# Kernel optimization log

Measured on AMD Instinct MI355X. Metric: run time of the kernel, lower is better.

## Reference

```python
import jax, jax.numpy as jnp
import numpy as np

B, A, D, H = 32, 64, 128, 512
F = A * D  # 8192

def setup_inputs() -> dict:
    key = jax.random.key(0)
    ks = jax.random.split(key, 20)
    s = 0.02
    return {
        "swarm_states": jax.random.normal(ks[0], (B, A, D), jnp.float32),
        "swarm_goals": jax.random.normal(ks[1], (B, A, D), jnp.float32),
        # quantum layer stand-in: Linear(F->F) + tanh
        "Wq": jax.random.normal(ks[2], (F, F), jnp.float32) * s,
        "bq": jnp.zeros((F,), jnp.float32),
        # interaction_net: Linear(2D->H) ReLU Linear(H->H) ReLU Linear(H->D)
        "Wi1": jax.random.normal(ks[3], (2 * D, H), jnp.float32) * s,
        "bi1": jnp.zeros((H,), jnp.float32),
        "Wi2": jax.random.normal(ks[4], (H, H), jnp.float32) * s,
        "bi2": jnp.zeros((H,), jnp.float32),
        "Wi3": jax.random.normal(ks[5], (H, D), jnp.float32) * s,
        "bi3": jnp.zeros((D,), jnp.float32),
        # coordination_net: Linear(F->H) ReLU Linear(H->H) ReLU Linear(H->F)
        "Wc1": jax.random.normal(ks[6], (F, H), jnp.float32) * s,
        "bc1": jnp.zeros((H,), jnp.float32),
        "Wc2": jax.random.normal(ks[7], (H, H), jnp.float32) * s,
        "bc2": jnp.zeros((H,), jnp.float32),
        "Wc3": jax.random.normal(ks[8], (H, F), jnp.float32) * s,
        "bc3": jnp.zeros((F,), jnp.float32),
    }

def reference(swarm_states, swarm_goals, Wq, bq, Wi1, bi1, Wi2, bi2, Wi3, bi3,
              Wc1, bc1, Wc2, bc2, Wc3, bc3):
    b, a, d = swarm_states.shape
    states_flat = swarm_states.reshape(b, a * d)
    # quantum feature extraction (stand-in for QuantumNeuralLayer)
    quantum_features = jnp.tanh(states_flat @ Wq + bq)  # (B, A*D)

    # vectorized pairwise interaction MLP over all ordered (i, j) pairs
    xi = jnp.broadcast_to(swarm_states[:, :, None, :], (b, a, a, d))
    xj = jnp.broadcast_to(swarm_states[:, None, :, :], (b, a, a, d))
    pair = jnp.concatenate([xi, xj], axis=-1)            # (B, A, A, 2D)
    h = jax.nn.relu(pair @ Wi1 + bi1)
    h = jax.nn.relu(h @ Wi2 + bi2)
    inter = h @ Wi3 + bi3                                # (B, A, A, D)
    offdiag = (1.0 - jnp.eye(a, dtype=inter.dtype))[None, :, :, None]
    # per-agent aggregation over the other agents (mean over j != i)
    interactions = (inter * offdiag).sum(axis=2) / (a - 1)  # (B, A, D)

    c = jax.nn.relu(quantum_features @ Wc1 + bc1)
    c = jax.nn.relu(c @ Wc2 + bc2)
    coordination = (c @ Wc3 + bc3).reshape(b, a, d)      # (B, A, D)

    coordinated_states = swarm_states + 0.1 * interactions + 0.1 * coordination
    return coordinated_states, quantum_features, interactions, coordination
```

## Files before the change

### kernel.cpp

```cpp
#include <hip/hip_runtime.h>

typedef __attribute__((ext_vector_type(8))) short bf16x8;
typedef __attribute__((ext_vector_type(16))) float f32x16;
typedef _Float16 f16;
typedef __attribute__((ext_vector_type(8))) _Float16 f16x8;

static __device__ __forceinline__ unsigned short f2bf(float x) {
  unsigned int u = __float_as_uint(x);
  return (unsigned short)((u + 0x7FFFu + ((u >> 16) & 1u)) >> 16);
}
static __device__ __forceinline__ unsigned int pk2bf(float lo, float hi) {
  return ((unsigned int)f2bf(hi) << 16) | f2bf(lo);
}

static __device__ __forceinline__ f16x8 relu8(f16x8 x) {
  f16x8 z = {0, 0, 0, 0, 0, 0, 0, 0};
  return __builtin_elementwise_max(x, z);
}

__global__ __launch_bounds__(256) void tobf_kernel(const float* __restrict__ src,
                                                   unsigned short* __restrict__ dst) {
  const int idx = blockIdx.x * 256 + threadIdx.x;
  float4 v = ((const float4*)src)[idx];
  ushort4 o;
  o.x = f2bf(v.x); o.y = f2bf(v.y); o.z = f2bf(v.z); o.w = f2bf(v.w);
  ((ushort4*)dst)[idx] = o;
}

__global__ __launch_bounds__(256) void w2h_kernel(const float* __restrict__ Wi2,
                                                  f16* __restrict__ W2h) {
  __shared__ float tile[32][33];
  const int t = threadIdx.x;
  const int bk = blockIdx.x, bn = blockIdx.y;
  const int r = t >> 5, c = t & 31;
#pragma unroll
  for (int p = 0; p < 4; p++) {
    int rr = p * 8 + r;
    tile[rr][c] = Wi2[(bk * 32 + rr) * 512 + bn * 32 + c];
  }
  __syncthreads();
#pragma unroll
  for (int p = 0; p < 4; p++) {
    int rr = p * 8 + r;
    W2h[(bn * 32 + rr) * 512 + bk * 32 + c] = (f16)tile[c][rr];
  }
}

__global__ __launch_bounds__(256) void uvh_kernel(const float* __restrict__ S,
                                                  const float* __restrict__ Wi1,
                                                  const float* __restrict__ bi1,
                                                  f16* __restrict__ Uh, f16* __restrict__ Vg) {
  __shared__ float st[128][12];
  const int t = threadIdx.x;
  const int row0 = blockIdx.x * 8;
  for (int idx = t; idx < 1024; idx += 256) {
    int r = idx >> 7, k = idx & 127;
    st[k][r] = S[(row0 + r) * 128 + k];
  }
  __syncthreads();
  float au0[8], au1[8], av0[8], av1[8];
#pragma unroll
  for (int r = 0; r < 8; r++) { au0[r] = 0.f; au1[r] = 0.f; av0[r] = 0.f; av1[r] = 0.f; }
#pragma unroll 4
  for (int k = 0; k < 128; k++) {
    float wt0 = Wi1[k * 512 + t];
    float wt1 = Wi1[k * 512 + 256 + t];
    float wb0 = Wi1[(k + 128) * 512 + t];
    float wb1 = Wi1[(k + 128) * 512 + 256 + t];
    float4 sA = *(const float4*)&st[k][0];
    float4 sB = *(const float4*)&st[k][4];
    float s8[8] = {sA.x, sA.y, sA.z, sA.w, sB.x, sB.y, sB.z, sB.w};
#pragma unroll
    for (int r = 0; r < 8; r++) {
      au0[r] += s8[r] * wt0;
      au1[r] += s8[r] * wt1;
      av0[r] += s8[r] * wb0;
      av1[r] += s8[r] * wb1;
    }
  }
  const float b0 = bi1[t], b1 = bi1[256 + t];
  const int kb = t >> 3, rem = t & 7;
#pragma unroll
  for (int r = 0; r < 8; r++) {
    const int row = row0 + r;
    Uh[row * 512 + t]       = (f16)(au0[r] + b0);
    Uh[row * 512 + 256 + t] = (f16)(au1[r] + b1);
    const int j = row & 63, bb = row >> 6;
    Vg[bb * 32768 + kb * 512 + j * 8 + rem]          = (f16)av0[r];
    Vg[bb * 32768 + (kb + 32) * 512 + j * 8 + rem]   = (f16)av1[r];
  }
}

__global__ __launch_bounds__(256, 4) void gemmw(const unsigned short* __restrict__ Abf,
                                                const float* __restrict__ W,
                                                float* __restrict__ P,
                                                int K, int N, int L, int l4sh) {
  __shared__ __align__(16) unsigned short As[32 * 512];
  const int t = threadIdx.x;
  const int k0 = blockIdx.y * L;
  const int L4 = L >> 2;
  const int swzm = 2 * L - 1;
  for (int idx = t; idx < (L << 3); idx += 256) {
    int row = idx >> l4sh, k4 = idx & (L4 - 1);
    ushort4 a4 = *(const ushort4*)&Abf[(size_t)row * K + k0 + k4 * 4];
    int off = (row * 2 * L + k4 * 8) ^ (((row & 7) << 4) & swzm);
    *(ushort4*)((char*)As + off) = a4;
  }
  __syncthreads();
  const int lane = t & 63, w = t >> 6;
  const int lrow = lane & 31, lh = lane >> 5;
  const int col = blockIdx.x * 128 + w * 32 + lrow;
  f32x16 acc0, acc1;
#pragma unroll
  for (int r = 0; r < 16; r++) { acc0[r] = 0.f; acc1[r] = 0.f; }
  const float* Wp = W + (size_t)(k0 + lh * 8) * N + col;
  const int aswz = ((lrow & 7) << 4) & swzm;
  const int abase = lrow * 2 * L + lh * 16;
  const int nks = L >> 4;
  int ks = 0;
  for (; ks + 1 < nks; ks += 2) {
    float wv0[8], wv1[8];
#pragma unroll
    for (int jj = 0; jj < 8; jj++) wv0[jj] = Wp[(size_t)(ks * 16 + jj) * N];
#pragma unroll
    for (int jj = 0; jj < 8; jj++) wv1[jj] = Wp[(size_t)(ks * 16 + 16 + jj) * N];
    uint4 b0, b1;
    b0.x = pk2bf(wv0[0], wv0[1]); b0.y = pk2bf(wv0[2], wv0[3]);
    b0.z = pk2bf(wv0[4], wv0[5]); b0.w = pk2bf(wv0[6], wv0[7]);
    b1.x = pk2bf(wv1[0], wv1[1]); b1.y = pk2bf(wv1[2], wv1[3]);
    b1.z = pk2bf(wv1[4], wv1[5]); b1.w = pk2bf(wv1[6], wv1[7]);
    bf16x8 af0 = *(const bf16x8*)((const char*)As + ((abase + ks * 32) ^ aswz));
    bf16x8 af1 = *(const bf16x8*)((const char*)As + ((abase + ks * 32 + 32) ^ aswz));
    acc0 = __builtin_amdgcn_mfma_f32_32x32x16_bf16(af0, *(const bf16x8*)&b0, acc0, 0, 0, 0);
    acc1 = __builtin_amdgcn_mfma_f32_32x32x16_bf16(af1, *(const bf16x8*)&b1, acc1, 0, 0, 0);
  }
  if (ks < nks) {
    float wv0[8];
#pragma unroll
    for (int jj = 0; jj < 8; jj++) wv0[jj] = Wp[(size_t)(ks * 16 + jj) * N];
    uint4 b0;
    b0.x = pk2bf(wv0[0], wv0[1]); b0.y = pk2bf(wv0[2], wv0[3]);
    b0.z = pk2bf(wv0[4], wv0[5]); b0.w = pk2bf(wv0[6], wv0[7]);
    bf16x8 af0 = *(const bf16x8*)((const char*)As + ((abase + ks * 32) ^ aswz));
    acc0 = __builtin_amdgcn_mfma_f32_32x32x16_bf16(af0, *(const bf16x8*)&b0, acc0, 0, 0, 0);
  }
  float* Pr = P + (size_t)blockIdx.y * 32 * N + col;
#pragma unroll
  for (int r = 0; r < 16; r++) {
    int row = (r & 3) + 8 * (r >> 2) + 4 * lh;
    Pr[(size_t)row * N] = acc0[r] + acc1[r];
  }
}

__global__ __launch_bounds__(256) void reduce_kernel(const float* __restrict__ P,
                                                     const float* __restrict__ bias,
                                                     float* __restrict__ dst,
                                                     unsigned short* __restrict__ dstbf,
                                                     int lnN, int KS, int act, int wbf) {
  const int idx = blockIdx.x * 256 + threadIdx.x;
  const int N = 1 << lnN;
  const int m = idx >> lnN, n = idx & (N - 1);
  float s = 0.f;
#pragma unroll 8
  for (int p = 0; p < KS; p++) s += P[((size_t)(p * 32 + m) << lnN) + n];
  s += bias[n];
  if (act == 1) s = fmaxf(s, 0.f);
  else if (act == 2) s = tanhf(s);
  dst[idx] = s;
  if (wbf) dstbf[idx] = f2bf(s);
}

__global__ __launch_bounds__(512, 2) void inter7_kernel(const f16* __restrict__ Uh,
                                                        const f16* __restrict__ Vg,
                                                        const f16* __restrict__ W2h,
                                                        const float* __restrict__ bi2,
                                                        float* __restrict__ Hsum) {
  __shared__ __align__(16) f16 Bt[128 * 512];
  const int t = threadIdx.x;
  const int nq = blockIdx.x;

#pragma unroll
  for (int i = 0; i < 16; i++) {
    int idx = i * 512 + t;
    int n = idx >> 6, ch = idx & 63;
    f16x8 w8 = *(const f16x8*)&W2h[(size_t)(nq * 128 + n) * 512 + ch * 8];
    int off = (n * 1024 + ch * 16) ^ ((n & 15) << 4);
    *(f16x8*)((char*)Bt + off) = w8;
  }
  __syncthreads();

  const int w = t >> 6, lane = t & 63;
  const int ii = w & 1, tg = w >> 1;
  const int lrow = lane & 31, lh = lane >> 5;
  const char* Btc = (const char*)Bt;

  int bofs[4], bswz[4];
#pragma unroll
  for (int nf = 0; nf < 4; nf++) {
    int nr = nf * 32 + lrow;
    bofs[nf] = nr * 1024 + lh * 16;
    bswz[nf] = (nr & 15) << 4;
  }

  const int b = blockIdx.y >> 1;
  const f16* Vbase = Vg + (size_t)b * 32768 + lh * 512 + lrow * 8;

  for (int s = 0; s < 4; s++) {
    const int tid = blockIdx.y * 16 + tg * 4 + s;
    const int it = tid & 31;
    const f16* Ub = Uh + (size_t)(b * 64 + it * 2 + ii) * 512 + lh * 8;

    f32x16 acc[2][4];
#pragma unroll
    for (int mf = 0; mf < 2; mf++)
#pragma unroll
      for (int nf = 0; nf < 4; nf++)
#pragma unroll
        for (int r = 0; r < 16; r++) acc[mf][nf][r] = 0.f;

    f16x8 v0 = *(const f16x8*)(Vbase);
    f16x8 v1 = *(const f16x8*)(Vbase + 256);
    f16x8 u0 = *(const f16x8*)(Ub);
    f16x8 bf[4];
#pragma unroll
    for (int nf = 0; nf < 4; nf++) bf[nf] = *(const f16x8*)(Btc + (bofs[nf] ^ bswz[nf]));

#pragma unroll 4
    for (int kc = 0; kc < 512; kc += 16) {
      const int kn = (kc + 16) & 511;
      f16x8 v0n = *(const f16x8*)(Vbase + kn * 64);
      f16x8 v1n = *(const f16x8*)(Vbase + kn * 64 + 256);
      f16x8 u0n = *(const f16x8*)(Ub + kn);
      f16x8 bfn[4];
#pragma unroll
      for (int nf = 0; nf < 4; nf++)
        bfn[nf] = *(const f16x8*)(Btc + ((bofs[nf] + kn * 2) ^ bswz[nf]));
      f16x8 a0 = relu8(v0 + u0);
      f16x8 a1 = relu8(v1 + u0);
#pragma unroll
      for (int nf = 0; nf < 4; nf++) {
        acc[0][nf] = __builtin_amdgcn_mfma_f32_32x32x16_f16(a0, bf[nf], acc[0][nf], 0, 0, 0);
        acc[1][nf] = __builtin_amdgcn_mfma_f32_32x32x16_f16(a1, bf[nf], acc[1][nf], 0, 0, 0);
      }
      v0 = v0n; v1 = v1n; u0 = u0n;
#pragma unroll
      for (int nf = 0; nf < 4; nf++) bf[nf] = bfn[nf];
    }

    const int iglob = it * 2 + ii;
    const int mf_d = iglob >> 5;
    const int rd = iglob & 31;
    const int lh_d = (rd >> 2) & 1;
    const int r_d = (rd & 3) + 4 * (rd >> 3);
#pragma unroll
    for (int nf = 0; nf < 4; nf++) {
      const int col = nq * 128 + nf * 32 + lrow;
      const float b2 = bi2[col];
      float ssum = 0.f;
#pragma unroll
      for (int mf = 0; mf < 2; mf++)
#pragma unroll
        for (int r = 0; r < 16; r++) {
          float x = fmaxf(acc[mf][nf][r] + b2, 0.f);
          if (mf == mf_d && r == r_d && lh == lh_d) x = 0.f;
          ssum += x;
        }
      ssum += __shfl_xor(ssum, 32);
      if (lh == 0) Hsum[(size_t)(b * 64 + iglob) * 512 + col] = ssum;
    }
  }
}

__global__ __launch_bounds__(256) void k3_kernel(const float* __restrict__ Hsum,
                                                 const float* __restrict__ Wi3,
                                                 const float* __restrict__ bi3,
                                                 float* __restrict__ inter) {
  __shared__ float st[512][10];
  const int t = threadIdx.x;
  const int row0 = blockIdx.x * 8;
  for (int idx = t; idx < 4096; idx += 256) {
    int r = idx >> 9, k = idx & 511;
    st[k][r] = Hsum[(row0 + r) * 512 + k] * (1.0f / 63.0f);
  }
  __syncthreads();
  const int c = t & 63;
  const int rg = t >> 6;
  float a0[2] = {0.f, 0.f}, a1[2] = {0.f, 0.f};
#pragma unroll 4
  for (int k = 0; k < 512; k++) {
    float w0 = Wi3[k * 128 + c];
    float w1 = Wi3[k * 128 + 64 + c];
    float2 h = *(const float2*)&st[k][rg * 2];
    a0[0] += h.x * w0; a0[1] += h.y * w0;
    a1[0] += h.x * w1; a1[1] += h.y * w1;
  }
  float b0 = bi3[c], b1 = bi3[64 + c];
#pragma unroll
  for (int r = 0; r < 2; r++) {
    inter[(row0 + rg * 2 + r) * 128 + c]      = a0[r] + b0;
    inter[(row0 + rg * 2 + r) * 128 + 64 + c] = a1[r] + b1;
  }
}

__global__ __launch_bounds__(256) void combine_kernel(const float* __restrict__ S,
                                                      const float* __restrict__ inter,
                                                      const float* __restrict__ coord,
                                                      float* __restrict__ out0) {
  const int i = blockIdx.x * 256 + threadIdx.x;
  float4 s = ((const float4*)S)[i];
  float4 a = ((const float4*)inter)[i];
  float4 c = ((const float4*)coord)[i];
  float4 o;
  o.x = s.x + 0.1f * (a.x + c.x);
  o.y = s.y + 0.1f * (a.y + c.y);
  o.z = s.z + 0.1f * (a.z + c.z);
  o.w = s.w + 0.1f * (a.w + c.w);
  ((float4*)out0)[i] = o;
}

extern "C" void kernel_launch(void* const* d_in, const int* in_sizes, int n_in,
                              void* d_out, int out_size, void* d_ws, size_t ws_size,
                              hipStream_t stream) {
  const float* states = (const float*)d_in[0];
  const float* Wq  = (const float*)d_in[2];
  const float* bq  = (const float*)d_in[3];
  const float* Wi1 = (const float*)d_in[4];
  const float* bi1 = (const float*)d_in[5];
  const float* Wi2 = (const float*)d_in[6];
  const float* bi2 = (const float*)d_in[7];
  const float* Wi3 = (const float*)d_in[8];
  const float* bi3 = (const float*)d_in[9];
  const float* Wc1 = (const float*)d_in[10];
  const float* bc1 = (const float*)d_in[11];
  const float* Wc2 = (const float*)d_in[12];
  const float* bc2 = (const float*)d_in[13];
  const float* Wc3 = (const float*)d_in[14];
  const float* bc3 = (const float*)d_in[15];

  float* out   = (float*)d_out;
  float* out0  = out;
  float* qf    = out + 262144;
  float* inter = out + 524288;
  float* coord = out + 786432;

  char* ws = (char*)d_ws;
  float*          P    = (float*)(ws);
  f16*            Uh   = (f16*)(ws + ((size_t)16 << 20));
  f16*            Vg   = (f16*)(ws + ((size_t)19 << 20));
  f16*            W2h  = (f16*)(ws + ((size_t)22 << 20));
  float*          Hsum = (float*)(ws + ((size_t)23 << 20));
  unsigned short* Sbf  = (unsigned short*)(ws + ((size_t)27 << 20));
  unsigned short* qfbf = (unsigned short*)(ws + ((size_t)28 << 20));
  float*          c1   = (float*)(ws + ((size_t)29 << 20));
  float*          c2   = (float*)(ws + ((size_t)29 << 20) + (1 << 16));
  unsigned short* c1bf = (unsigned short*)(ws + ((size_t)29 << 20) + (2 << 16));
  unsigned short* c2bf = (unsigned short*)(ws + ((size_t)29 << 20) + (3 << 16));

  tobf_kernel<<<256, 256, 0, stream>>>(states, Sbf);
  w2h_kernel<<<dim3(16, 16), 256, 0, stream>>>(Wi2, W2h);
  uvh_kernel<<<256, 256, 0, stream>>>(states, Wi1, bi1, Uh, Vg);

  gemmw<<<dim3(64, 16), 256, 0, stream>>>(Sbf, Wq, P, 8192, 8192, 512, 7);
  reduce_kernel<<<1024, 256, 0, stream>>>(P, bq, qf, qfbf, 13, 16, 2, 1);

  inter7_kernel<<<dim3(4, 64), 512, 0, stream>>>(Uh, Vg, W2h, bi2, Hsum);
  k3_kernel<<<256, 256, 0, stream>>>(Hsum, Wi3, bi3, inter);

  gemmw<<<dim3(4, 64), 256, 0, stream>>>(qfbf, Wc1, P, 8192, 512, 128, 5);
  reduce_kernel<<<64, 256, 0, stream>>>(P, bc1, c1, c1bf, 9, 64, 1, 1);
  gemmw<<<dim3(4, 32), 256, 0, stream>>>(c1bf, Wc2, P, 512, 512, 16, 2);
  reduce_kernel<<<64, 256, 0, stream>>>(P, bc2, c2, c2bf, 9, 32, 1, 1);
  gemmw<<<dim3(64, 8), 256, 0, stream>>>(c2bf, Wc3, P, 512, 8192, 64, 4);
  reduce_kernel<<<1024, 256, 0, stream>>>(P, bc3, coord, qfbf, 13, 8, 0, 0);

  combine_kernel<<<256, 256, 0, stream>>>(states, inter, coord, out0);
}
```

Baseline: 233.3 us.

## Halve pairwise-MLP N tile and re-layout LDS weights for higher occupancy

The pairwise interaction kernel now handles 64 output columns per block instead of 128, so it uses half the LDS (64KB) and half the accumulators, and raises launch bounds to 4 blocks per CU. The grid doubles to 8 column blocks. The W2 tile is stored in LDS in a k-major, MFMA-fragment-friendly layout with no XOR swizzle, which makes addressing simpler. In exchange, the relu(U+V) A-operand is recomputed twice as often across blocks and V/U global reads double.

```diff
diff --git a/kernel.cpp b/kernel.cpp
--- a/kernel.cpp
+++ b/kernel.cpp
@@ -170,21 +170,21 @@
   if (wbf) dstbf[idx] = f2bf(s);
 }
 
-__global__ __launch_bounds__(512, 2) void inter7_kernel(const f16* __restrict__ Uh,
+__global__ __launch_bounds__(512, 4) void inter8_kernel(const f16* __restrict__ Uh,
                                                         const f16* __restrict__ Vg,
                                                         const f16* __restrict__ W2h,
                                                         const float* __restrict__ bi2,
                                                         float* __restrict__ Hsum) {
-  __shared__ __align__(16) f16 Bt[128 * 512];
+  __shared__ __align__(16) f16 Bt[32 * 1024];
   const int t = threadIdx.x;
   const int nq = blockIdx.x;
 
 #pragma unroll
-  for (int i = 0; i < 16; i++) {
+  for (int i = 0; i < 8; i++) {
     int idx = i * 512 + t;
     int n = idx >> 6, ch = idx & 63;
-    f16x8 w8 = *(const f16x8*)&W2h[(size_t)(nq * 128 + n) * 512 + ch * 8];
-    int off = (n * 1024 + ch * 16) ^ ((n & 15) << 4);
+    f16x8 w8 = *(const f16x8*)&W2h[(size_t)(nq * 64 + n) * 512 + ch * 8];
+    int off = (ch >> 1) * 2048 + (ch & 1) * 1024 + n * 16;
     *(f16x8*)((char*)Bt + off) = w8;
   }
   __syncthreads();
@@ -194,13 +194,8 @@
   const int lrow = lane & 31, lh = lane >> 5;
   const char* Btc = (const char*)Bt;
 
-  int bofs[4], bswz[4];
-#pragma unroll
-  for (int nf = 0; nf < 4; nf++) {
-    int nr = nf * 32 + lrow;
-    bofs[nf] = nr * 1024 + lh * 16;
-    bswz[nf] = (nr & 15) << 4;
-  }
+  const int bbase0 = lh * 1024 + lrow * 16;
+  const int bbase1 = bbase0 + 512;
 
   const int b = blockIdx.y >> 1;
   const f16* Vbase = Vg + (size_t)b * 32768 + lh * 512 + lrow * 8;
@@ -210,41 +205,31 @@
     const int it = tid & 31;
     const f16* Ub = Uh + (size_t)(b * 64 + it * 2 + ii) * 512 + lh * 8;
 
-    f32x16 acc[2][4];
-#pragma unroll
-    for (int mf = 0; mf < 2; mf++)
-#pragma unroll
-      for (int nf = 0; nf < 4; nf++)
-#pragma unroll
-        for (int r = 0; r < 16; r++) acc[mf][nf][r] = 0.f;
+    f32x16 acc00, acc01, acc10, acc11;
+#pragma unroll
+    for (int r = 0; r < 16; r++) { acc00[r] = 0.f; acc01[r] = 0.f; acc10[r] = 0.f; acc11[r] = 0.f; }
 
     f16x8 v0 = *(const f16x8*)(Vbase);
     f16x8 v1 = *(const f16x8*)(Vbase + 256);
     f16x8 u0 = *(const f16x8*)(Ub);
-    f16x8 bf[4];
-#pragma unroll
-    for (int nf = 0; nf < 4; nf++) bf[nf] = *(const f16x8*)(Btc + (bofs[nf] ^ bswz[nf]));
+    f16x8 bf0 = *(const f16x8*)(Btc + bbase0);
+    f16x8 bf1 = *(const f16x8*)(Btc + bbase1);
 
 #pragma unroll 4
-    for (int kc = 0; kc < 512; kc += 16) {
-      const int kn = (kc + 16) & 511;
-      f16x8 v0n = *(const f16x8*)(Vbase + kn * 64);
-      f16x8 v1n = *(const f16x8*)(Vbase + kn * 64 + 256);
-      f16x8 u0n = *(const f16x8*)(Ub + kn);
-      f16x8 bfn[4];
-#pragma unroll
-      for (int nf = 0; nf < 4; nf++)
-        bfn[nf] = *(const f16x8*)(Btc + ((bofs[nf] + kn * 2) ^ bswz[nf]));
+    for (int ks = 0; ks < 32; ks++) {
+      const int kn = (ks + 1) & 31;
+      f16x8 v0n = *(const f16x8*)(Vbase + kn * 1024);
+      f16x8 v1n = *(const f16x8*)(Vbase + kn * 1024 + 256);
+      f16x8 u0n = *(const f16x8*)(Ub + kn * 16);
+      f16x8 bf0n = *(const f16x8*)(Btc + (kn * 2048 + bbase0));
+      f16x8 bf1n = *(const f16x8*)(Btc + (kn * 2048 + bbase1));
       f16x8 a0 = relu8(v0 + u0);
       f16x8 a1 = relu8(v1 + u0);
-#pragma unroll
-      for (int nf = 0; nf < 4; nf++) {
-        acc[0][nf] = __builtin_amdgcn_mfma_f32_32x32x16_f16(a0, bf[nf], acc[0][nf], 0, 0, 0);
-        acc[1][nf] = __builtin_amdgcn_mfma_f32_32x32x16_f16(a1, bf[nf], acc[1][nf], 0, 0, 0);
-      }
-      v0 = v0n; v1 = v1n; u0 = u0n;
-#pragma unroll
-      for (int nf = 0; nf < 4; nf++) bf[nf] = bfn[nf];
+      acc00 = __builtin_amdgcn_mfma_f32_32x32x16_f16(a0, bf0, acc00, 0, 0, 0);
+      acc01 = __builtin_amdgcn_mfma_f32_32x32x16_f16(a0, bf1, acc01, 0, 0, 0);
+      acc10 = __builtin_amdgcn_mfma_f32_32x32x16_f16(a1, bf0, acc10, 0, 0, 0);
+      acc11 = __builtin_amdgcn_mfma_f32_32x32x16_f16(a1, bf1, acc11, 0, 0, 0);
+      v0 = v0n; v1 = v1n; u0 = u0n; bf0 = bf0n; bf1 = bf1n;
     }
 
     const int iglob = it * 2 + ii;
@@ -253,18 +238,18 @@
     const int lh_d = (rd >> 2) & 1;
     const int r_d = (rd & 3) + 4 * (rd >> 3);
 #pragma unroll
-    for (int nf = 0; nf < 4; nf++) {
-      const int col = nq * 128 + nf * 32 + lrow;
+    for (int nf = 0; nf < 2; nf++) {
+      const int col = nq * 64 + nf * 32 + lrow;
       const float b2 = bi2[col];
       float ssum = 0.f;
 #pragma unroll
-      for (int mf = 0; mf < 2; mf++)
-#pragma unroll
-        for (int r = 0; r < 16; r++) {
-          float x = fmaxf(acc[mf][nf][r] + b2, 0.f);
-          if (mf == mf_d && r == r_d && lh == lh_d) x = 0.f;
-          ssum += x;
-        }
+      for (int r = 0; r < 16; r++) {
+        float x0 = fmaxf((nf ? acc01[r] : acc00[r]) + b2, 0.f);
+        float x1 = fmaxf((nf ? acc11[r] : acc10[r]) + b2, 0.f);
+        if (mf_d == 0 && r == r_d && lh == lh_d) x0 = 0.f;
+        if (mf_d == 1 && r == r_d && lh == lh_d) x1 = 0.f;
+        ssum += x0 + x1;
+      }
       ssum += __shfl_xor(ssum, 32);
       if (lh == 0) Hsum[(size_t)(b * 64 + iglob) * 512 + col] = ssum;
     }
@@ -363,7 +348,7 @@
   gemmw<<<dim3(64, 16), 256, 0, stream>>>(Sbf, Wq, P, 8192, 8192, 512, 7);
   reduce_kernel<<<1024, 256, 0, stream>>>(P, bq, qf, qfbf, 13, 16, 2, 1);
 
-  inter7_kernel<<<dim3(4, 64), 512, 0, stream>>>(Uh, Vg, W2h, bi2, Hsum);
+  inter8_kernel<<<dim3(8, 64), 512, 0, stream>>>(Uh, Vg, W2h, bi2, Hsum);
   k3_kernel<<<256, 256, 0, stream>>>(Hsum, Wi3, bi3, inter);
 
   gemmw<<<dim3(4, 64), 256, 0, stream>>>(qfbf, Wc1, P, 8192, 512, 128, 5);
```

Measured after the change: 241.0 us. 1.03x slower.
